# Optimization experiments

Hardware: AMD Instinct MI355X
Metric: run time of the kernel (lower is better)

Reference implementation:

```python
import jax, jax.numpy as jnp
import numpy as np

B = 4096
D = 512
TEMPERATURE = 0.07


def setup_inputs() -> dict:
    key = jax.random.key(0)
    k1, k2 = jax.random.split(key)
    logits = jax.random.normal(k1, (B, D), dtype=jnp.float32)
    label = jax.random.normal(k2, (B, D), dtype=jnp.float32)
    return {"logits": logits, "label": label}


def reference(logits, label):
    # concat the two views -> [2B, D]
    feats = jnp.concatenate([logits, label], axis=0)
    n = feats.shape[0]
    b = n // 2
    # L2 normalize along feature dim (F.normalize, eps for safety)
    norm = jnp.maximum(jnp.linalg.norm(feats, axis=1, keepdims=True), 1e-12)
    feats = feats / norm
    # similarity matrix [2B, 2B]
    sim = jnp.matmul(feats, feats.T) / TEMPERATURE
    idx = jnp.arange(n)
    # positive pair of row i is row (i + B) mod 2B
    pos = sim[idx, (idx + b) % n]
    # CrossEntropy with target 0 over [pos, negatives] == masked LSE - pos.
    # Mask out the diagonal (self-similarity), which the torch code removes
    # via the boolean-eye mask before building logits.
    neg_inf = jnp.array(-jnp.inf, dtype=sim.dtype)
    sim_masked = jnp.where(idx[:, None] == idx[None, :], neg_inf, sim)
    lse = jax.nn.logsumexp(sim_masked, axis=1)
    loss = jnp.mean(lse - pos)
    return loss
```

## Files before the change

### kernel.cpp

```cpp
#include <hip/hip_runtime.h>
#include <hip/hip_bf16.h>

#define NROWS 8192
#define BHALF 4096
#define DDIM  512

#define BM 256
#define BK 64
#define KT (DDIM / BK)
#define NT (NROWS / BM)
#define NTRI (NT * (NT + 1) / 2)
#define CPX (NTRI / 8)

#define FSCALE 3.7796447300922722f

typedef short bf16x8 __attribute__((ext_vector_type(8)));
typedef float f32x4 __attribute__((ext_vector_type(4)));
typedef unsigned short u16x8 __attribute__((ext_vector_type(8)));
typedef __attribute__((address_space(1))) unsigned int gu32;
typedef __attribute__((address_space(3))) unsigned int lu32;

#define MFMA_(a, b, c) __builtin_amdgcn_mfma_f32_16x16x32_bf16(a, b, c, 0, 0, 0)
#define VMCNT(N) asm volatile("s_waitcnt vmcnt(" #N ")" ::: "memory")
#define LGKM0                                            \
  do {                                                   \
    asm volatile("s_waitcnt lgkmcnt(0)" ::: "memory");   \
    __builtin_amdgcn_sched_barrier(0);                   \
  } while (0)
#define BAR                                              \
  do {                                                   \
    __builtin_amdgcn_sched_barrier(0);                   \
    __builtin_amdgcn_s_barrier();                        \
    __builtin_amdgcn_sched_barrier(0);                   \
  } while (0)

__global__ __launch_bounds__(256) void normalize_kernel(
    const float* __restrict__ logits, const float* __restrict__ label,
    unsigned short* __restrict__ fn, float* __restrict__ rowsum,
    float* __restrict__ out) {
  if (blockIdx.x < 8)
    ((float4*)rowsum)[blockIdx.x * 256 + threadIdx.x] =
        make_float4(0.f, 0.f, 0.f, 0.f);
  if (blockIdx.x == 8 && threadIdx.x == 0) out[0] = 0.f;

  const int w = threadIdx.x >> 6, lane = threadIdx.x & 63;
  const int row = blockIdx.x * 4 + w;
  const float* src = (row < BHALF) ? (logits + (size_t)row * DDIM)
                                   : (label + (size_t)(row - BHALF) * DDIM);
  const float4* s4 = (const float4*)src;
  float4 a = s4[lane * 2 + 0];
  float4 b = s4[lane * 2 + 1];
  float ss = a.x * a.x + a.y * a.y + a.z * a.z + a.w * a.w +
             b.x * b.x + b.y * b.y + b.z * b.z + b.w * b.w;
#pragma unroll
  for (int m = 1; m < 64; m <<= 1) ss += __shfl_xor(ss, m);
  const float inv = FSCALE / fmaxf(sqrtf(ss), 1e-12f);
  const float v[8] = {a.x, a.y, a.z, a.w, b.x, b.y, b.z, b.w};
  u16x8 o;
#pragma unroll
  for (int j = 0; j < 8; ++j) {
    float x = v[j] * inv;
    unsigned u = __float_as_uint(x);
    unsigned r = (u + 0x7fffu + ((u >> 16) & 1u)) >> 16;
    o[j] = (unsigned short)r;
  }
  *(u16x8*)(fn + (size_t)row * DDIM + lane * 8) = o;
}

__global__ __launch_bounds__(512) void simexp_tri_kernel(
    const unsigned short* __restrict__ fn, float* __restrict__ rowsum,
    float* __restrict__ pos) {
  extern __shared__ char lds[];
  __shared__ float lds_rsum[BM];
  __shared__ float lds_csum[BM];

  const int bid0 = (int)blockIdx.x;
  const int bid = (bid0 & 7) * CPX + (bid0 >> 3);
  const int u = (NTRI - 1) - bid;
  int k = (int)((sqrtf(8.f * (float)u + 1.f) - 1.f) * 0.5f);
  while ((k + 1) * (k + 2) / 2 <= u) ++k;
  while (k * (k + 1) / 2 > u) --k;
  const int rm = (NT - 1) - k;
  const int cn = (NT - 1) - (u - k * (k + 1) / 2);
  const int rowBase = rm * BM, colBase = cn * BM;
  const bool diag = (rm == cn);
  const bool posTile = (cn == rm + NT / 2);

  const int tid = threadIdx.x;
  const int w = tid >> 6, lane = tid & 63;
  const int wr = w >> 2, wc = w & 3;
  const int l15 = lane & 15, l4 = lane >> 4;

  if (tid < BM) { lds_rsum[tid] = 0.f; lds_csum[tid] = 0.f; }

  const int r8 = lane >> 3;
  const int sw16 = ((lane & 7) ^ r8) << 4;

  auto stageA = [&](int d, int kk, int R) {
    const char* g =
        (const char*)(fn + (size_t)(rowBase + R + w * 8 + r8) * DDIM + kk) + sw16;
    __builtin_amdgcn_global_load_lds(
        (gu32*)g, (lu32*)(lds + d * 65536 + (R + w * 8) * 128), 16, 0, 0);
  };
  auto stageB = [&](int d, int kk, int R) {
    const char* g =
        (const char*)(fn + (size_t)(colBase + R + w * 8 + r8) * DDIM + kk) + sw16;
    __builtin_amdgcn_global_load_lds(
        (gu32*)g, (lu32*)(lds + d * 65536 + 32768 + (R + w * 8) * 128), 16, 0, 0);
  };
  auto readA = [&](int d, int m, int ks) -> bf16x8 {
    const int r = wr * 128 + m * 16 + l15;
    return *(const bf16x8*)(lds + d * 65536 + r * 128 +
                            (((ks * 4 + l4) ^ (r & 7)) << 4));
  };
  auto readB = [&](int d, int n, int ks) -> bf16x8 {
    const int r = wc * 64 + n * 16 + l15;
    return *(const bf16x8*)(lds + d * 65536 + 32768 + r * 128 +
                            (((ks * 4 + l4) ^ (r & 7)) << 4));
  };

  f32x4 acc[8][4];
#pragma unroll
  for (int m = 0; m < 8; ++m)
#pragma unroll
    for (int n = 0; n < 4; ++n) acc[m][n] = (f32x4){0.f, 0.f, 0.f, 0.f};

#define PHASE0(STAGES)                                                    \
  {                                                                       \
    _Pragma("unroll") for (int n = 0; n < 4; ++n) {                       \
      bf[n][0] = readB(d, n, 0);                                          \
      bf[n][1] = readB(d, n, 1);                                          \
    }                                                                     \
    bf16x8 a00 = readA(d, 0, 0), a01 = readA(d, 0, 1);                    \
    bf16x8 a10 = readA(d, 1, 0), a11 = readA(d, 1, 1);                    \
    STAGES;                                                               \
    BAR;                                                                  \
    LGKM0;                                                                \
    __builtin_amdgcn_s_setprio(1);                                        \
    _Pragma("unroll") for (int n = 0; n < 4; ++n) {                       \
      acc[0][n] = MFMA_(a00, bf[n][0], acc[0][n]);                        \
      acc[1][n] = MFMA_(a10, bf[n][0], acc[1][n]);                        \
    }                                                                     \
    _Pragma("unroll") for (int n = 0; n < 4; ++n) {                       \
      acc[0][n] = MFMA_(a01, bf[n][1], acc[0][n]);                        \
      acc[1][n] = MFMA_(a11, bf[n][1], acc[1][n]);                        \
    }                                                                     \
    __builtin_amdgcn_s_setprio(0);                                        \
    BAR;                                                                  \
  }

#define PHASE(P, STAGES, TAILWAIT)                                        \
  {                                                                       \
    bf16x8 a00 = readA(d, 2 * (P), 0), a01 = readA(d, 2 * (P), 1);        \
    bf16x8 a10 = readA(d, 2 * (P) + 1, 0), a11 = readA(d, 2 * (P) + 1, 1);\
    STAGES;                                                               \
    BAR;                                                                  \
    LGKM0;                                                                \
    __builtin_amdgcn_s_setprio(1);                                        \
    _Pragma("unroll") for (int n = 0; n < 4; ++n) {                       \
      acc[2 * (P)][n] = MFMA_(a00, bf[n][0], acc[2 * (P)][n]);            \
      acc[2 * (P) + 1][n] = MFMA_(a10, bf[n][0], acc[2 * (P) + 1][n]);    \
    }                                                                     \
    _Pragma("unroll") for (int n = 0; n < 4; ++n) {                       \
      acc[2 * (P)][n] = MFMA_(a01, bf[n][1], acc[2 * (P)][n]);            \
      acc[2 * (P) + 1][n] = MFMA_(a11, bf[n][1], acc[2 * (P) + 1][n]);    \
    }                                                                     \
    __builtin_amdgcn_s_setprio(0);                                        \
    TAILWAIT;                                                             \
    BAR;                                                                  \
  }

  stageB(0, 0, 0);  stageB(0, 0, 64); stageB(0, 0, 128); stageB(0, 0, 192);
  stageA(0, 0, 0);  stageA(0, 0, 128);
  stageA(0, 0, 64); stageA(0, 0, 192);
  VMCNT(2);
  BAR;

  for (int t = 0; t < KT - 1; ++t) {
    const int d = t & 1, o = d ^ 1;
    const int kn = (t + 1) * BK;
    bf16x8 bf[4][2];
    PHASE0(stageB(o, kn, 0); stageB(o, kn, 64));
    PHASE(1, stageB(o, kn, 128); stageB(o, kn, 192), VMCNT(4));
    PHASE(2, stageA(o, kn, 0); stageA(o, kn, 128), (void)0);
    PHASE(3, stageA(o, kn, 64); stageA(o, kn, 192), VMCNT(2));
  }
  {
    const int d = (KT - 1) & 1;
    bf16x8 bf[4][2];
    PHASE0((void)0);
    PHASE(1, (void)0, VMCNT(0));
    PHASE(2, (void)0, (void)0);
    PHASE(3, (void)0, (void)0);
  }
#undef PHASE0
#undef PHASE

  float rs[8][4];
  float cs[4];
#pragma unroll
  for (int m = 0; m < 8; ++m)
#pragma unroll
    for (int j = 0; j < 4; ++j) rs[m][j] = 0.f;
#pragma unroll
  for (int n = 0; n < 4; ++n) cs[n] = 0.f;

#pragma unroll
  for (int m = 0; m < 8; ++m)
#pragma unroll
    for (int n = 0; n < 4; ++n)
#pragma unroll
      for (int j = 0; j < 4; ++j) {
        const int rl = wr * 128 + m * 16 + l4 * 4 + j;
        const int cl = wc * 64 + n * 16 + l15;
        const float v = acc[m][n][j];
        float e = __expf(v);
        if (diag && rl == cl) e = 0.f;
        rs[m][j] += e;
        cs[n] += e;
        if (posTile && rl == cl) pos[rowBase + rl] = v;
      }

#pragma unroll
  for (int m = 0; m < 8; ++m)
#pragma unroll
    for (int j = 0; j < 4; ++j) {
      float s = rs[m][j];
      s += __shfl_xor(s, 1);
      s += __shfl_xor(s, 2);
      s += __shfl_xor(s, 4);
      s += __shfl_xor(s, 8);
      if (l15 == 0)
        atomicAdd(&lds_rsum[wr * 128 + m * 16 + l4 * 4 + j], s);
    }
  if (!diag) {
#pragma unroll
    for (int n = 0; n < 4; ++n) {
      float s = cs[n];
      s += __shfl_xor(s, 16);
      s += __shfl_xor(s, 32);
      if (l4 == 0) atomicAdd(&lds_csum[wc * 64 + n * 16 + l15], s);
    }
  }
  __syncthreads();
  if (tid < BM) {
    atomicAdd(&rowsum[rowBase + tid], lds_rsum[tid]);
    if (!diag) atomicAdd(&rowsum[colBase + tid], lds_csum[tid]);
  }
}

__global__ __launch_bounds__(256) void reduce_kernel(
    const float* __restrict__ rowsum, const float* __restrict__ pos,
    float* __restrict__ out) {
  __shared__ float part[4];
  const int i = blockIdx.x * 256 + threadIdx.x;
  float a = __logf(rowsum[i]) - pos[i & (BHALF - 1)];
#pragma unroll
  for (int m = 1; m < 64; m <<= 1) a += __shfl_xor(a, m);
  const int w = threadIdx.x >> 6, lane = threadIdx.x & 63;
  if (lane == 0) part[w] = a;
  __syncthreads();
  if (threadIdx.x == 0)
    atomicAdd(out, (part[0] + part[1] + part[2] + part[3]) * (1.0f / NROWS));
}

extern "C" void kernel_launch(void* const* d_in, const int* in_sizes, int n_in,
                              void* d_out, int out_size, void* d_ws, size_t ws_size,
                              hipStream_t stream) {
  const float* logits = (const float*)d_in[0];
  const float* label = (const float*)d_in[1];
  float* out = (float*)d_out;
  unsigned short* fn = (unsigned short*)d_ws;
  float* rowsum = (float*)((char*)d_ws + (size_t)NROWS * DDIM * 2);
  float* pos = rowsum + NROWS;

  normalize_kernel<<<NROWS / 4, 256, 0, stream>>>(logits, label, fn, rowsum, out);
  simexp_tri_kernel<<<NTRI, 512, 2 * 65536, stream>>>(fn, rowsum, pos);
  reduce_kernel<<<NROWS / 256, 256, 0, stream>>>(rowsum, pos, out);
}
```

Measured before the change: 129.4 us.

## Split tail tiles into half-width tiles and fuse final reduction via last-block counter

The triangular tile grid (528 tiles of 256x256) is re-partitioned into 512 full tiles plus 16 tiles split into 32 half-width (256x128) blocks, so the last wave is better balanced across CUs. Diagonal/positive masking is now computed from global indices so half tiles work. The separate reduce kernel is removed; a global atomic counter lets the last finishing block compute the log-sum and mean, saving a launch. This adds a threadfence and atomic per block and a serialized single-block tail reduction.

```diff
diff --git a/kernel.cpp b/kernel.cpp
--- a/kernel.cpp
+++ b/kernel.cpp
@@ -10,7 +10,9 @@
 #define KT (DDIM / BK)
 #define NT (NROWS / BM)
 #define NTRI (NT * (NT + 1) / 2)
-#define CPX (NTRI / 8)
+#define NFULL 512
+#define NHALFB 32
+#define GRID (NFULL + NHALFB)
 
 #define FSCALE 3.7796447300922722f
 
@@ -36,12 +38,11 @@
 
 __global__ __launch_bounds__(256) void normalize_kernel(
     const float* __restrict__ logits, const float* __restrict__ label,
-    unsigned short* __restrict__ fn, float* __restrict__ rowsum,
-    float* __restrict__ out) {
+    unsigned short* __restrict__ fn, float* __restrict__ rowsum, int* ctr) {
   if (blockIdx.x < 8)
     ((float4*)rowsum)[blockIdx.x * 256 + threadIdx.x] =
         make_float4(0.f, 0.f, 0.f, 0.f);
-  if (blockIdx.x == 8 && threadIdx.x == 0) out[0] = 0.f;
+  if (blockIdx.x == 8 && threadIdx.x == 0) *ctr = 0;
 
   const int w = threadIdx.x >> 6, lane = threadIdx.x & 63;
   const int row = blockIdx.x * 4 + w;
@@ -67,32 +68,16 @@
   *(u16x8*)(fn + (size_t)row * DDIM + lane * 8) = o;
 }
 
-__global__ __launch_bounds__(512) void simexp_tri_kernel(
-    const unsigned short* __restrict__ fn, float* __restrict__ rowsum,
-    float* __restrict__ pos) {
-  extern __shared__ char lds[];
-  __shared__ float lds_rsum[BM];
-  __shared__ float lds_csum[BM];
-
-  const int bid0 = (int)blockIdx.x;
-  const int bid = (bid0 & 7) * CPX + (bid0 >> 3);
-  const int u = (NTRI - 1) - bid;
-  int k = (int)((sqrtf(8.f * (float)u + 1.f) - 1.f) * 0.5f);
-  while ((k + 1) * (k + 2) / 2 <= u) ++k;
-  while (k * (k + 1) / 2 > u) --k;
-  const int rm = (NT - 1) - k;
-  const int cn = (NT - 1) - (u - k * (k + 1) / 2);
-  const int rowBase = rm * BM, colBase = cn * BM;
-  const bool diag = (rm == cn);
-  const bool posTile = (cn == rm + NT / 2);
-
+template <int BN_>
+__device__ void tile_pipeline(const unsigned short* __restrict__ fn,
+                              float* __restrict__ rowsum,
+                              float* __restrict__ pos, int rowBase, int colBase,
+                              char* lds, float* lds_rsum, float* lds_csum) {
+  constexpr int NFRAG = BN_ / 64;
   const int tid = threadIdx.x;
   const int w = tid >> 6, lane = tid & 63;
   const int wr = w >> 2, wc = w & 3;
   const int l15 = lane & 15, l4 = lane >> 4;
-
-  if (tid < BM) { lds_rsum[tid] = 0.f; lds_csum[tid] = 0.f; }
-
   const int r8 = lane >> 3;
   const int sw16 = ((lane & 7) ^ r8) << 4;
 
@@ -114,20 +99,20 @@
                             (((ks * 4 + l4) ^ (r & 7)) << 4));
   };
   auto readB = [&](int d, int n, int ks) -> bf16x8 {
-    const int r = wc * 64 + n * 16 + l15;
+    const int r = wc * (BN_ / 4) + n * 16 + l15;
     return *(const bf16x8*)(lds + d * 65536 + 32768 + r * 128 +
                             (((ks * 4 + l4) ^ (r & 7)) << 4));
   };
 
-  f32x4 acc[8][4];
+  f32x4 acc[8][NFRAG];
 #pragma unroll
   for (int m = 0; m < 8; ++m)
 #pragma unroll
-    for (int n = 0; n < 4; ++n) acc[m][n] = (f32x4){0.f, 0.f, 0.f, 0.f};
+    for (int n = 0; n < NFRAG; ++n) acc[m][n] = (f32x4){0.f, 0.f, 0.f, 0.f};
 
 #define PHASE0(STAGES)                                                    \
   {                                                                       \
-    _Pragma("unroll") for (int n = 0; n < 4; ++n) {                       \
+    _Pragma("unroll") for (int n = 0; n < NFRAG; ++n) {                   \
       bf[n][0] = readB(d, n, 0);                                          \
       bf[n][1] = readB(d, n, 1);                                          \
     }                                                                     \
@@ -137,11 +122,11 @@
     BAR;                                                                  \
     LGKM0;                                                                \
     __builtin_amdgcn_s_setprio(1);                                        \
-    _Pragma("unroll") for (int n = 0; n < 4; ++n) {                       \
+    _Pragma("unroll") for (int n = 0; n < NFRAG; ++n) {                   \
       acc[0][n] = MFMA_(a00, bf[n][0], acc[0][n]);                        \
       acc[1][n] = MFMA_(a10, bf[n][0], acc[1][n]);                        \
     }                                                                     \
-    _Pragma("unroll") for (int n = 0; n < 4; ++n) {                       \
+    _Pragma("unroll") for (int n = 0; n < NFRAG; ++n) {                   \
       acc[0][n] = MFMA_(a01, bf[n][1], acc[0][n]);                        \
       acc[1][n] = MFMA_(a11, bf[n][1], acc[1][n]);                        \
     }                                                                     \
@@ -157,11 +142,11 @@
     BAR;                                                                  \
     LGKM0;                                                                \
     __builtin_amdgcn_s_setprio(1);                                        \
-    _Pragma("unroll") for (int n = 0; n < 4; ++n) {                       \
+    _Pragma("unroll") for (int n = 0; n < NFRAG; ++n) {                   \
       acc[2 * (P)][n] = MFMA_(a00, bf[n][0], acc[2 * (P)][n]);            \
       acc[2 * (P) + 1][n] = MFMA_(a10, bf[n][0], acc[2 * (P) + 1][n]);    \
     }                                                                     \
-    _Pragma("unroll") for (int n = 0; n < 4; ++n) {                       \
+    _Pragma("unroll") for (int n = 0; n < NFRAG; ++n) {                   \
       acc[2 * (P)][n] = MFMA_(a01, bf[n][1], acc[2 * (P)][n]);            \
       acc[2 * (P) + 1][n] = MFMA_(a11, bf[n][1], acc[2 * (P) + 1][n]);    \
     }                                                                     \
@@ -170,24 +155,35 @@
     BAR;                                                                  \
   }
 
-  stageB(0, 0, 0);  stageB(0, 0, 64); stageB(0, 0, 128); stageB(0, 0, 192);
-  stageA(0, 0, 0);  stageA(0, 0, 128);
-  stageA(0, 0, 64); stageA(0, 0, 192);
+  stageB(0, 0, 0);
+  stageB(0, 0, 64);
+  if constexpr (BN_ == 256) {
+    stageB(0, 0, 128);
+    stageB(0, 0, 192);
+  }
+  stageA(0, 0, 0);
+  stageA(0, 0, 128);
+  stageA(0, 0, 64);
+  stageA(0, 0, 192);
   VMCNT(2);
   BAR;
 
   for (int t = 0; t < KT - 1; ++t) {
     const int d = t & 1, o = d ^ 1;
     const int kn = (t + 1) * BK;
-    bf16x8 bf[4][2];
+    bf16x8 bf[NFRAG][2];
     PHASE0(stageB(o, kn, 0); stageB(o, kn, 64));
-    PHASE(1, stageB(o, kn, 128); stageB(o, kn, 192), VMCNT(4));
+    if constexpr (BN_ == 256) {
+      PHASE(1, stageB(o, kn, 128); stageB(o, kn, 192), VMCNT(4));
+    } else {
+      PHASE(1, (void)0, VMCNT(2));
+    }
     PHASE(2, stageA(o, kn, 0); stageA(o, kn, 128), (void)0);
     PHASE(3, stageA(o, kn, 64); stageA(o, kn, 192), VMCNT(2));
   }
   {
     const int d = (KT - 1) & 1;
-    bf16x8 bf[4][2];
+    bf16x8 bf[NFRAG][2];
     PHASE0((void)0);
     PHASE(1, (void)0, VMCNT(0));
     PHASE(2, (void)0, (void)0);
@@ -197,28 +193,29 @@
 #undef PHASE
 
   float rs[8][4];
-  float cs[4];
+  float cs[NFRAG];
 #pragma unroll
   for (int m = 0; m < 8; ++m)
 #pragma unroll
     for (int j = 0; j < 4; ++j) rs[m][j] = 0.f;
 #pragma unroll
-  for (int n = 0; n < 4; ++n) cs[n] = 0.f;
+  for (int n = 0; n < NFRAG; ++n) cs[n] = 0.f;
 
 #pragma unroll
   for (int m = 0; m < 8; ++m)
 #pragma unroll
-    for (int n = 0; n < 4; ++n)
+    for (int n = 0; n < NFRAG; ++n)
 #pragma unroll
       for (int j = 0; j < 4; ++j) {
         const int rl = wr * 128 + m * 16 + l4 * 4 + j;
-        const int cl = wc * 64 + n * 16 + l15;
+        const int cl = wc * (BN_ / 4) + n * 16 + l15;
+        const int grow = rowBase + rl, gcol = colBase + cl;
         const float v = acc[m][n][j];
         float e = __expf(v);
-        if (diag && rl == cl) e = 0.f;
+        if (grow == gcol) e = 0.f;
         rs[m][j] += e;
         cs[n] += e;
-        if (posTile && rl == cl) pos[rowBase + rl] = v;
+        if (gcol == grow + BHALF) pos[grow] = v;
       }
 
 #pragma unroll
@@ -230,38 +227,89 @@
       s += __shfl_xor(s, 2);
       s += __shfl_xor(s, 4);
       s += __shfl_xor(s, 8);
-      if (l15 == 0)
-        atomicAdd(&lds_rsum[wr * 128 + m * 16 + l4 * 4 + j], s);
+      if (l15 == 0) atomicAdd(&lds_rsum[wr * 128 + m * 16 + l4 * 4 + j], s);
     }
-  if (!diag) {
-#pragma unroll
-    for (int n = 0; n < 4; ++n) {
+  if (rowBase != colBase) {
+#pragma unroll
+    for (int n = 0; n < NFRAG; ++n) {
       float s = cs[n];
       s += __shfl_xor(s, 16);
       s += __shfl_xor(s, 32);
-      if (l4 == 0) atomicAdd(&lds_csum[wc * 64 + n * 16 + l15], s);
+      if (l4 == 0) atomicAdd(&lds_csum[wc * (BN_ / 4) + n * 16 + l15], s);
     }
   }
   __syncthreads();
+  if (tid < BM) atomicAdd(&rowsum[rowBase + tid], lds_rsum[tid]);
+  if (rowBase != colBase && tid < BN_)
+    atomicAdd(&rowsum[colBase + tid], lds_csum[tid]);
+}
+
+__global__ __launch_bounds__(512) void simexp_tri_kernel(
+    const unsigned short* __restrict__ fn, float* __restrict__ rowsum,
+    float* __restrict__ pos, int* __restrict__ ctr, float* __restrict__ out) {
+  extern __shared__ char lds[];
+  __shared__ float lds_rsum[BM];
+  __shared__ float lds_csum[BM];
+  __shared__ int is_last;
+
+  const int bid = (int)blockIdx.x;
+  const bool half = (bid >= NFULL);
+  int beta, colOff = 0;
+  if (!half) {
+    const int b = (bid & 7) * (NFULL / 8) + (bid >> 3);
+    beta = (b == 1) ? 527 : b;
+  } else {
+    const int hb = bid - NFULL;
+    const int t = NFULL + (hb >> 1);
+    beta = (t == 527) ? 1 : t;
+    colOff = (hb & 1) * 128;
+  }
+  int k = (int)((sqrtf(8.f * (float)beta + 1.f) - 1.f) * 0.5f);
+  while ((k + 1) * (k + 2) / 2 <= beta) ++k;
+  while (k * (k + 1) / 2 > beta) --k;
+  const int rm = (NT - 1) - k;
+  const int cn = (NT - 1) - (beta - k * (k + 1) / 2);
+  const int rowBase = rm * BM, colBase = cn * BM + colOff;
+
+  const int tid = threadIdx.x;
   if (tid < BM) {
-    atomicAdd(&rowsum[rowBase + tid], lds_rsum[tid]);
-    if (!diag) atomicAdd(&rowsum[colBase + tid], lds_csum[tid]);
-  }
-}
-
-__global__ __launch_bounds__(256) void reduce_kernel(
-    const float* __restrict__ rowsum, const float* __restrict__ pos,
-    float* __restrict__ out) {
-  __shared__ float part[4];
-  const int i = blockIdx.x * 256 + threadIdx.x;
-  float a = __logf(rowsum[i]) - pos[i & (BHALF - 1)];
+    lds_rsum[tid] = 0.f;
+    lds_csum[tid] = 0.f;
+  }
+
+  if (!half)
+    tile_pipeline<256>(fn, rowsum, pos, rowBase, colBase, lds, lds_rsum, lds_csum);
+  else
+    tile_pipeline<128>(fn, rowsum, pos, rowBase, colBase, lds, lds_rsum, lds_csum);
+
+  __threadfence();
+  if (tid == 0) {
+    const int done = __hip_atomic_fetch_add(ctr, 1, __ATOMIC_ACQ_REL,
+                                            __HIP_MEMORY_SCOPE_AGENT);
+    is_last = (done == GRID - 1);
+  }
+  __syncthreads();
+  if (!is_last) return;
+
+  float a = 0.f;
+  for (int i = tid; i < NROWS; i += 512) {
+    const float r = __hip_atomic_load(&rowsum[i], __ATOMIC_RELAXED,
+                                      __HIP_MEMORY_SCOPE_AGENT);
+    const float p = __hip_atomic_load(&pos[i & (BHALF - 1)], __ATOMIC_RELAXED,
+                                      __HIP_MEMORY_SCOPE_AGENT);
+    a += __logf(r) - p;
+  }
 #pragma unroll
   for (int m = 1; m < 64; m <<= 1) a += __shfl_xor(a, m);
-  const int w = threadIdx.x >> 6, lane = threadIdx.x & 63;
-  if (lane == 0) part[w] = a;
+  const int w = tid >> 6, lane = tid & 63;
+  if (lane == 0) lds_rsum[w] = a;
   __syncthreads();
-  if (threadIdx.x == 0)
-    atomicAdd(out, (part[0] + part[1] + part[2] + part[3]) * (1.0f / NROWS));
+  if (tid == 0) {
+    float t = 0.f;
+#pragma unroll
+    for (int i = 0; i < 8; ++i) t += lds_rsum[i];
+    out[0] = t * (1.0f / NROWS);
+  }
 }
 
 extern "C" void kernel_launch(void* const* d_in, const int* in_sizes, int n_in,
@@ -273,8 +321,8 @@
   unsigned short* fn = (unsigned short*)d_ws;
   float* rowsum = (float*)((char*)d_ws + (size_t)NROWS * DDIM * 2);
   float* pos = rowsum + NROWS;
-
-  normalize_kernel<<<NROWS / 4, 256, 0, stream>>>(logits, label, fn, rowsum, out);
-  simexp_tri_kernel<<<NTRI, 512, 2 * 65536, stream>>>(fn, rowsum, pos);
-  reduce_kernel<<<NROWS / 256, 256, 0, stream>>>(rowsum, pos, out);
+  int* ctr = (int*)(pos + BHALF);
+
+  normalize_kernel<<<NROWS / 4, 256, 0, stream>>>(logits, label, fn, rowsum, ctr);
+  simexp_tri_kernel<<<GRID, 512, 2 * 65536, stream>>>(fn, rowsum, pos, ctr, out);
 }
```

After: 296.9 us. 2.29x slower.
